# Kernel optimization log

Measured on AMD Instinct MI355X. Metric: run time of the kernel, lower is better.

## Reference

```python
import jax, jax.numpy as jnp
import numpy as np

D = 256; NH = 8; NL = 4; NP = 4; DFF = 1024
SHAPES = [(100, 100), (50, 50), (25, 25), (13, 13)]
B = 4


def layer_norm(x, g, b, eps=1e-5):
    m = x.mean(-1, keepdims=True)
    v = ((x - m) ** 2).mean(-1, keepdims=True)
    return (x - m) * jax.lax.rsqrt(v + eps) * g + b


def setup_inputs() -> dict:
    key = jax.random.key(0)
    ks = jax.random.split(key, 12)
    Lin = sum(h * w for h, w in SHAPES)  # 13294
    w = lambda k, s: jax.random.normal(k, s, jnp.float32) * 0.02
    return dict(
        src=jax.random.normal(ks[0], (B, Lin, D), jnp.float32),
        pos=0.1 * jax.random.normal(ks[1], (B, Lin, D), jnp.float32),
        reference_points=jax.random.uniform(ks[2], (B, Lin, NL, 2), dtype=jnp.float32),
        spatial_shapes=jnp.array(SHAPES, jnp.int32),
        level_start_index=jnp.array(np.cumsum([0] + [h * w for h, w in SHAPES])[:-1], jnp.int32),
        value_w=w(ks[3], (D, D)), value_b=jnp.zeros((D,), jnp.float32),
        offs_w=w(ks[4], (D, NH * NL * NP * 2)),
        offs_b=0.5 * jax.random.normal(ks[5], (NH * NL * NP * 2,), jnp.float32),
        attn_w=w(ks[6], (D, NH * NL * NP)), attn_b=jnp.zeros((NH * NL * NP,), jnp.float32),
        out_w=w(ks[7], (D, D)), out_b=jnp.zeros((D,), jnp.float32),
        ln1_g=jnp.ones((D,), jnp.float32), ln1_b=jnp.zeros((D,), jnp.float32),
        ff1_w=w(ks[8], (D, DFF)), ff1_b=jnp.zeros((DFF,), jnp.float32),
        ff2_w=w(ks[9], (DFF, D)), ff2_b=jnp.zeros((D,), jnp.float32),
        ln2_g=jnp.ones((D,), jnp.float32), ln2_b=jnp.zeros((D,), jnp.float32),
    )


def msda(query, value_in, ref, shapes, starts, value_w, value_b, offs_w, offs_b,
         attn_w, attn_b, out_w, out_b):
    Bq, Lq, Dm = query.shape
    dh = Dm // NH
    shapes_np = np.asarray(shapes); starts_np = np.asarray(starts)
    value = (value_in @ value_w + value_b).reshape(Bq, -1, NH, dh)
    offs = (query @ offs_w + offs_b).reshape(Bq, Lq, NH, NL, NP, 2)
    aw = jax.nn.softmax((query @ attn_w + attn_b).reshape(Bq, Lq, NH, NL * NP), axis=-1)
    aw = aw.reshape(Bq, Lq, NH, NL, NP)
    # offset normalizer is (W, H) per level
    normalizer = jnp.stack([shapes[:, 1], shapes[:, 0]], -1).astype(jnp.float32)
    loc = ref[:, :, None, :, None, :] + offs / normalizer[None, None, None, :, None, :]
    out = jnp.zeros((Bq, NH, Lq, dh), jnp.float32)
    for l in range(NL):
        Hl, Wl = int(shapes_np[l, 0]), int(shapes_np[l, 1])
        s = int(starts_np[l])
        v = value[:, s:s + Hl * Wl].transpose(0, 2, 1, 3)  # [B,h,HW,dh]
        x = loc[:, :, :, l, :, 0] * Wl - 0.5  # [B,Lq,h,P], align_corners=False
        y = loc[:, :, :, l, :, 1] * Hl - 0.5
        x0 = jnp.floor(x); y0 = jnp.floor(y)
        dx = x - x0; dy = y - y0
        x0i = x0.astype(jnp.int32); y0i = y0.astype(jnp.int32)
        def gather(ix, iy):
            valid = (ix >= 0) & (ix < Wl) & (iy >= 0) & (iy < Hl)  # zero padding
            idx = jnp.clip(iy, 0, Hl - 1) * Wl + jnp.clip(ix, 0, Wl - 1)
            idx = idx.transpose(0, 2, 1, 3).reshape(Bq, NH, Lq * NP)
            g = jnp.take_along_axis(v, idx[..., None], axis=2).reshape(Bq, NH, Lq, NP, dh)
            return g * valid.transpose(0, 2, 1, 3)[..., None]
        dxh = dx.transpose(0, 2, 1, 3)[..., None]
        dyh = dy.transpose(0, 2, 1, 3)[..., None]
        sampled = (gather(x0i, y0i) * (1 - dxh) * (1 - dyh)
                   + gather(x0i + 1, y0i) * dxh * (1 - dyh)
                   + gather(x0i, y0i + 1) * (1 - dxh) * dyh
                   + gather(x0i + 1, y0i + 1) * dxh * dyh)  # [B,h,Lq,P,dh]
        awl = aw[:, :, :, l].transpose(0, 2, 1, 3)[..., None]  # [B,h,Lq,P,1]
        out = out + (sampled * awl).sum(3)
    out = out.transpose(0, 2, 1, 3).reshape(Bq, Lq, Dm)
    return out @ out_w + out_b


def reference(src, pos, reference_points, spatial_shapes, level_start_index,
              value_w, value_b, offs_w, offs_b, attn_w, attn_b, out_w, out_b,
              ln1_g, ln1_b, ff1_w, ff1_b, ff2_w, ff2_b, ln2_g, ln2_b):
    # src = with_pos_embed(src, pos): NOTE this module uses (src + pos) as BOTH query and value
    q = src + pos
    src2 = msda(q, q, reference_points, spatial_shapes, level_start_index,
                value_w, value_b, offs_w, offs_b, attn_w, attn_b, out_w, out_b)
    x = layer_norm(q + src2, ln1_g, ln1_b)  # dropout is identity at eval
    ff = jnp.maximum(x @ ff1_w + ff1_b, 0.0) @ ff2_w + ff2_b
    return layer_norm(x + ff, ln2_g, ln2_b)
```

## Files before the change

### kernel.cpp

```cpp
#include <hip/hip_runtime.h>
#include <hip/hip_bf16.h>

#define B_    4
#define LIN   13294
#define M_    (B_*LIN)
#define D_    256
#define NH_   8
#define NL_   4
#define NP_   4
#define DFF_  1024

typedef __bf16 bf16;
typedef unsigned int uint;
typedef __attribute__((ext_vector_type(8))) __bf16 bfrag8;
typedef __attribute__((ext_vector_type(4))) __bf16 bf16x4;
typedef __attribute__((ext_vector_type(4))) float facc4;
typedef __attribute__((ext_vector_type(2))) float f32x2;

__global__ __launch_bounds__(256) void make_q(const float* __restrict__ src,
                                              const float* __restrict__ pos,
                                              float* __restrict__ q,
                                              bf16* __restrict__ qb, int n4) {
  int i = blockIdx.x * 256 + threadIdx.x;
  if (i >= n4) return;
  float4 s = ((const float4*)src)[i];
  float4 p = ((const float4*)pos)[i];
  float4 v = {s.x + p.x, s.y + p.y, s.z + p.z, s.w + p.w};
  ((float4*)q)[i] = v;
  bf16 t4[4] = {(bf16)v.x, (bf16)v.y, (bf16)v.z, (bf16)v.w};
  ((uint2*)qb)[i] = *(uint2*)t4;
}

__global__ __launch_bounds__(256) void prep_weights(
    const float* __restrict__ vw, const float* __restrict__ ow,
    const float* __restrict__ aw, const float* __restrict__ outw,
    const float* __restrict__ f1w, const float* __restrict__ f2w,
    const float* __restrict__ vb, const float* __restrict__ ob,
    const float* __restrict__ ab,
    bf16* __restrict__ vowt, bf16* __restrict__ outwt,
    bf16* __restrict__ f1wt, bf16* __restrict__ f2wt, float* __restrict__ vobias) {
  int seg = blockIdx.y;
  int idx = blockIdx.x * 256 + threadIdx.x;
  if (seg == 6) {
    if (idx < 256) vobias[idx] = vb[idx];
    else if (idx < 512) vobias[idx] = ob[idx - 256];
    else if (idx < 640) vobias[idx] = ab[idx - 512];
    return;
  }
  const float* W; bf16* Wt; int K, N;
  switch (seg) {
    case 0: W = vw;   Wt = vowt;              K = 256;  N = 256;  break;
    case 1: W = ow;   Wt = vowt + 256 * 256;  K = 256;  N = 256;  break;
    case 2: W = aw;   Wt = vowt + 512 * 256;  K = 256;  N = 128;  break;
    case 3: W = outw; Wt = outwt;             K = 256;  N = 256;  break;
    case 4: W = f1w;  Wt = f1wt;              K = 256;  N = 1024; break;
    default: W = f2w; Wt = f2wt;              K = 1024; N = 256;  break;
  }
  if (idx < K * N) {
    int n = idx / K, k = idx - n * K;
    Wt[idx] = (bf16)W[k * N + n];
  }
}

__device__ __forceinline__ void gload16(const bf16* g, bf16* l) {
  __builtin_amdgcn_global_load_lds(
      (const __attribute__((address_space(1))) uint*)g,
      (__attribute__((address_space(3))) uint*)l, 16, 0, 0);
}

template<int K, bool RELU>
__global__ __launch_bounds__(256) void gemm128(
    const bf16* __restrict__ A, const bf16* __restrict__ Bt,
    const float* __restrict__ bias, bf16* __restrict__ C,
    int Mdim, int N) {
  __shared__ __align__(16) bf16 As[128 * 64];
  __shared__ __align__(16) bf16 Bs[128 * 64];
  const int t = threadIdx.x, wave = t >> 6, lane = t & 63;
  const int m0 = blockIdx.x * 128, n0 = blockIdx.y * 128;
  const int wr = wave >> 1, wc = wave & 1;
  const int ln = lane & 15, quad = lane >> 4;
  const int sr = lane >> 3, cc = lane & 7;
  const int gcol = (cc ^ sr) * 8;

  const bf16* ap[4]; const bf16* bp[4];
  bf16* la[4]; bf16* lb[4];
  #pragma unroll
  for (int ii = 0; ii < 4; ii++) {
    int i = wave * 4 + ii;
    int arow = min(m0 + i * 8 + sr, Mdim - 1);
    ap[ii] = A + (size_t)arow * K + gcol;
    bp[ii] = Bt + (size_t)(n0 + i * 8 + sr) * K + gcol;
    la[ii] = As + i * 512;
    lb[ii] = Bs + i * 512;
  }
  int a_off[4], b_off[4];
  #pragma unroll
  for (int i = 0; i < 4; i++) {
    int ra = wr * 64 + i * 16 + ln;
    int rb = wc * 64 + i * 16 + ln;
    a_off[i] = ra * 128 + ((quad ^ (ra & 7)) * 16);
    b_off[i] = rb * 128 + ((quad ^ (rb & 7)) * 16);
  }

  facc4 acc[4][4];
  #pragma unroll
  for (int mt = 0; mt < 4; mt++)
    #pragma unroll
    for (int nt = 0; nt < 4; nt++) acc[mt][nt] = (facc4){0.f, 0.f, 0.f, 0.f};

  #pragma unroll 1
  for (int k0 = 0; k0 < K; k0 += 64) {
    __syncthreads();
    gload16(ap[0] + k0, la[0]); gload16(ap[1] + k0, la[1]);
    gload16(ap[2] + k0, la[2]); gload16(ap[3] + k0, la[3]);
    gload16(bp[0] + k0, lb[0]); gload16(bp[1] + k0, lb[1]);
    gload16(bp[2] + k0, lb[2]); gload16(bp[3] + k0, lb[3]);
    __syncthreads();
    #pragma unroll
    for (int ks = 0; ks < 2; ks++) {
      bfrag8 wfr[4], xfr[4];
      #pragma unroll
      for (int nt = 0; nt < 4; nt++)
        wfr[nt] = *(const bfrag8*)((const char*)Bs + (b_off[nt] ^ (ks * 64)));
      #pragma unroll
      for (int mt = 0; mt < 4; mt++)
        xfr[mt] = *(const bfrag8*)((const char*)As + (a_off[mt] ^ (ks * 64)));
      #pragma unroll
      for (int mt = 0; mt < 4; mt++)
        #pragma unroll
        for (int nt = 0; nt < 4; nt++)
          acc[mt][nt] = __builtin_amdgcn_mfma_f32_16x16x32_bf16(wfr[nt], xfr[mt], acc[mt][nt], 0, 0, 0);
    }
  }

  #pragma unroll
  for (int nt = 0; nt < 4; nt++) {
    int ncol = n0 + wc * 64 + nt * 16 + quad * 4;
    float4 bv = *(const float4*)&bias[ncol];
    #pragma unroll
    for (int mt = 0; mt < 4; mt++) {
      int row = m0 + wr * 64 + mt * 16 + ln;
      if (row < Mdim) {
        float v0 = acc[mt][nt][0] + bv.x, v1 = acc[mt][nt][1] + bv.y;
        float v2 = acc[mt][nt][2] + bv.z, v3 = acc[mt][nt][3] + bv.w;
        if (RELU) {
          v0 = fmaxf(v0, 0.f); v1 = fmaxf(v1, 0.f);
          v2 = fmaxf(v2, 0.f); v3 = fmaxf(v3, 0.f);
        }
        bf16 o[4] = {(bf16)v0, (bf16)v1, (bf16)v2, (bf16)v3};
        *(uint2*)&C[(size_t)row * N + ncol] = *(uint2*)o;
      }
    }
  }
}

__global__ __launch_bounds__(256) void msda_sample(
    const bf16* __restrict__ VOA,
    const float* __restrict__ ref,
    bf16* __restrict__ sampled) {
  int gw = (blockIdx.x * 256 + threadIdx.x) >> 6;
  int lane = threadIdx.x & 63;
  int m = gw >> 3, h = gw & 7;
  if (m >= M_) return;
  int b = m / LIN;
  int p = lane >> 2, cg = lane & 3;
  int l = p >> 2, pt = p & 3;
  int Wl = (l == 0) ? 100 : (l == 1) ? 50 : (l == 2) ? 25 : 13;
  int Hl = Wl;
  int st = (l == 0) ? 0 : (l == 1) ? 10000 : (l == 2) ? 12500 : 13125;

  const bf16* row = VOA + (size_t)m * 640;
  float e = __expf((float)row[512 + h * 16 + p]);
  float se = e;
  #pragma unroll
  for (int msk = 4; msk < 64; msk <<= 1) se += __shfl_xor(se, msk);
  float w = e / se;

  float rx = ref[((size_t)m * 4 + l) * 2 + 0];
  float ry = ref[((size_t)m * 4 + l) * 2 + 1];
  uint oxy = *(const uint*)&row[256 + ((h * 4 + l) * 4 + pt) * 2];
  float ox = __uint_as_float(oxy << 16);
  float oy = __uint_as_float(oxy & 0xffff0000u);
  float x = rx * (float)Wl + ox - 0.5f;
  float y = ry * (float)Hl + oy - 0.5f;
  float x0f = floorf(x), y0f = floorf(y);
  float dx = x - x0f, dy = y - y0f;
  int x0 = (int)x0f, y0 = (int)y0f;
  float wx1 = 1.f - dx, wy1 = 1.f - dy;

  f32x2 acc2[4];
  #pragma unroll
  for (int i = 0; i < 4; i++) acc2[i] = (f32x2){0.f, 0.f};

  size_t vbase = ((size_t)(b * LIN + st)) * 640 + h * 32 + cg * 8;
  #pragma unroll
  for (int c = 0; c < 4; c++) {
    int cx = c & 1, cy = c >> 1;
    int xi = x0 + cx, yi = y0 + cy;
    bool valid = (xi >= 0) & (xi < Wl) & (yi >= 0) & (yi < Hl);
    int xc = min(max(xi, 0), Wl - 1);
    int yc = min(max(yi, 0), Hl - 1);
    float cw = (cx ? dx : wx1) * (cy ? dy : wy1) * w;
    cw = valid ? cw : 0.f;
    uint off = (uint)(yc * Wl + xc) * 640u;
    const uint4 vv = *(const uint4*)(VOA + vbase + off);
    f32x2 cw2 = {cw, cw};
    f32x2 v0 = {__uint_as_float(vv.x << 16), __uint_as_float(vv.x & 0xffff0000u)};
    f32x2 v1 = {__uint_as_float(vv.y << 16), __uint_as_float(vv.y & 0xffff0000u)};
    f32x2 v2 = {__uint_as_float(vv.z << 16), __uint_as_float(vv.z & 0xffff0000u)};
    f32x2 v3 = {__uint_as_float(vv.w << 16), __uint_as_float(vv.w & 0xffff0000u)};
    acc2[0] = cw2 * v0 + acc2[0];
    acc2[1] = cw2 * v1 + acc2[1];
    acc2[2] = cw2 * v2 + acc2[2];
    acc2[3] = cw2 * v3 + acc2[3];
  }

  int sel = (lane >> 2) & 1;
  f32x2 sA0 = sel ? acc2[0] : acc2[2];
  f32x2 sA1 = sel ? acc2[1] : acc2[3];
  f32x2 kA0 = sel ? acc2[2] : acc2[0];
  f32x2 kA1 = sel ? acc2[3] : acc2[1];
  f32x2 rA0, rA1;
  rA0.x = __shfl_xor(sA0.x, 4); rA0.y = __shfl_xor(sA0.y, 4);
  rA1.x = __shfl_xor(sA1.x, 4); rA1.y = __shfl_xor(sA1.y, 4);
  kA0 += rA0; kA1 += rA1;

  int sel2 = (lane >> 3) & 1;
  f32x2 sB = sel2 ? kA0 : kA1;
  f32x2 kB = sel2 ? kA1 : kA0;
  f32x2 rB;
  rB.x = __shfl_xor(sB.x, 8); rB.y = __shfl_xor(sB.y, 8);
  kB += rB;

  int sel3 = (lane >> 4) & 1;
  float sC = sel3 ? kB.x : kB.y;
  float kC = sel3 ? kB.y : kB.x;
  kC += __shfl_xor(sC, 16);

  float v = kC + __shfl_xor(kC, 32);

  if (lane < 32) {
    int c = cg * 8 + ((lane >> 2) & 1) * 4 + ((lane >> 3) & 1) * 2 + ((lane >> 4) & 1);
    sampled[(size_t)m * 256 + h * 32 + c] = (bf16)v;
  }
}

__device__ inline float4 load4f(const float* p) { return *(const float4*)p; }
__device__ inline float4 load4f(const bf16* p) {
  bf16x4 v = *(const bf16x4*)p;
  float4 r = {(float)v[0], (float)v[1], (float)v[2], (float)v[3]};
  return r;
}
template<typename RT>
__global__ __launch_bounds__(256) void ln_kernel(
    const bf16* __restrict__ a, const RT* __restrict__ res,
    const float* __restrict__ g, const float* __restrict__ beta,
    float* __restrict__ out_f, bf16* __restrict__ out_b, int Mdim) {
  int wave = threadIdx.x >> 6, lane = threadIdx.x & 63;
  int row = blockIdx.x * 4 + wave;
  if (row >= Mdim) return;
  size_t base = (size_t)row * 256 + lane * 4;
  float4 av = load4f(a + base);
  float4 rv = load4f(res + base);
  float4 v = {av.x + rv.x, av.y + rv.y, av.z + rv.z, av.w + rv.w};
  float s = v.x + v.y + v.z + v.w;
  #pragma unroll
  for (int msk = 1; msk < 64; msk <<= 1) s += __shfl_xor(s, msk);
  float mean = s * (1.f / 256.f);
  float4 d = {v.x - mean, v.y - mean, v.z - mean, v.w - mean};
  float sq = d.x * d.x + d.y * d.y + d.z * d.z + d.w * d.w;
  #pragma unroll
  for (int msk = 1; msk < 64; msk <<= 1) sq += __shfl_xor(sq, msk);
  float inv = rsqrtf(sq * (1.f / 256.f) + 1e-5f);
  float4 gv = *(const float4*)(g + lane * 4);
  float4 bv = *(const float4*)(beta + lane * 4);
  float4 y = {d.x * inv * gv.x + bv.x, d.y * inv * gv.y + bv.y,
              d.z * inv * gv.z + bv.z, d.w * inv * gv.w + bv.w};
  if (out_f) *(float4*)(out_f + base) = y;
  if (out_b) {
    bf16 t4[4] = {(bf16)y.x, (bf16)y.y, (bf16)y.z, (bf16)y.w};
    *(uint2*)(out_b + base) = *(uint2*)t4;
  }
}

extern "C" void kernel_launch(void* const* d_in, const int* in_sizes, int n_in,
                              void* d_out, int out_size, void* d_ws, size_t ws_size,
                              hipStream_t stream) {
  const float* src     = (const float*)d_in[0];
  const float* pos     = (const float*)d_in[1];
  const float* refpts  = (const float*)d_in[2];
  const float* value_w = (const float*)d_in[5];
  const float* value_b = (const float*)d_in[6];
  const float* offs_w  = (const float*)d_in[7];
  const float* offs_b  = (const float*)d_in[8];
  const float* attn_w  = (const float*)d_in[9];
  const float* attn_b  = (const float*)d_in[10];
  const float* out_w   = (const float*)d_in[11];
  const float* out_b   = (const float*)d_in[12];
  const float* ln1_g   = (const float*)d_in[13];
  const float* ln1_b   = (const float*)d_in[14];
  const float* ff1_w   = (const float*)d_in[15];
  const float* ff1_b   = (const float*)d_in[16];
  const float* ff2_w   = (const float*)d_in[17];
  const float* ff2_b   = (const float*)d_in[18];
  const float* ln2_g   = (const float*)d_in[19];
  const float* ln2_b   = (const float*)d_in[20];

  char* ws = (char*)d_ws;
  size_t off = 0;
  auto take = [&](size_t bytes) -> char* {
    char* pp = ws + off;
    off += (bytes + 255) & ~(size_t)255;
    return pp;
  };
  float* q      = (float*)take((size_t)M_ * 256 * 4);
  size_t szQB   = (size_t)M_ * 256 * 2;
  size_t szVOA  = (size_t)M_ * 640 * 2;
  char* R       = take(szQB + szVOA + szQB);
  bf16* qb      = (bf16*)R;
  bf16* VOA     = (bf16*)(R + szQB);
  bf16* sampled = (bf16*)(R + szQB + szVOA);
  bf16* hb      = (bf16*)R;
  bf16* tmp     = (bf16*)take(szQB);
  bf16* x       = (bf16*)take(szQB);
  bf16* vowt    = (bf16*)take(640 * 256 * 2);
  bf16* outwt   = (bf16*)take(65536 * 2);
  bf16* f1wt    = (bf16*)take(262144 * 2);
  bf16* f2wt    = (bf16*)take(262144 * 2);
  float* vobias = (float*)take(640 * 4);
  (void)ws_size; (void)in_sizes; (void)n_in; (void)out_size;

  int n4 = M_ * 256 / 4;
  make_q<<<dim3((n4 + 255) / 256), dim3(256), 0, stream>>>(src, pos, q, qb, n4);
  prep_weights<<<dim3(1024, 7), dim3(256), 0, stream>>>(
      value_w, offs_w, attn_w, out_w, ff1_w, ff2_w, value_b, offs_b, attn_b,
      vowt, outwt, f1wt, f2wt, vobias);

  dim3 blk(256);
  int mt = (M_ + 127) / 128;
  gemm128<256, false><<<dim3(mt, 5), blk, 0, stream>>>(qb, vowt, vobias, VOA, M_, 640);
  msda_sample<<<dim3(M_ * 2), blk, 0, stream>>>(VOA, refpts, sampled);
  gemm128<256, false><<<dim3(mt, 2), blk, 0, stream>>>(sampled, outwt, out_b, tmp, M_, 256);
  ln_kernel<float><<<dim3((M_ + 3) / 4), blk, 0, stream>>>(tmp, q, ln1_g, ln1_b, nullptr, x, M_);
  gemm128<256, true><<<dim3(mt, 8), blk, 0, stream>>>(x, f1wt, ff1_b, hb, M_, 1024);
  gemm128<1024, false><<<dim3(mt, 2), blk, 0, stream>>>(hb, f2wt, ff2_b, tmp, M_, 256);
  ln_kernel<bf16><<<dim3((M_ + 3) / 4), blk, 0, stream>>>(tmp, x, ln2_g, ln2_b, (float*)d_out, nullptr, M_);
}
```

Baseline: 590.0 us.

## Assign one bilinear corner per lane and reduce sampled values through LDS

Each lane of the MSDA sampling kernel now handles one bilinear corner of one sample point. It loads the full 32-channel head slice as four 16-byte loads, where before each lane covered an 8-channel group across all four corners. Partial products go to a padded shared-memory buffer, are summed by column reads, and then reduced across lanes with xor shuffles. The aim is to cut the serial dependent gather loop and the select-heavy shuffle reduction, and to make each lane's loads contiguous. The cost is LDS traffic, a bigger per-lane register footprint, and inline waitcnt asm that relies on wave-synchronous execution.

```diff
diff --git a/kernel.cpp b/kernel.cpp
--- a/kernel.cpp
+++ b/kernel.cpp
@@ -154,16 +154,49 @@
   }
 }
 
+__device__ __forceinline__ f32x2 bfpair(uint u, f32x2 s) {
+  f32x2 r = {__uint_as_float(u << 16), __uint_as_float(u & 0xffff0000u)};
+  return r * s;
+}
+
+__device__ __forceinline__ void msda_phase(
+    uint4 A, uint4 B, f32x2 cw2, float* lrow, const float* rb,
+    bf16* outp, int lane) {
+  f32x2* lp = (f32x2*)lrow;
+  lp[0] = bfpair(A.x, cw2); lp[1] = bfpair(A.y, cw2);
+  lp[2] = bfpair(A.z, cw2); lp[3] = bfpair(A.w, cw2);
+  lp[4] = bfpair(B.x, cw2); lp[5] = bfpair(B.y, cw2);
+  lp[6] = bfpair(B.z, cw2); lp[7] = bfpair(B.w, cw2);
+  asm volatile("s_waitcnt lgkmcnt(0)" ::: "memory");
+  f32x2 s0 = *(const f32x2*)(rb + 0 * 18) + *(const f32x2*)(rb + 1 * 18);
+  f32x2 s1 = *(const f32x2*)(rb + 2 * 18) + *(const f32x2*)(rb + 3 * 18);
+  f32x2 s2 = *(const f32x2*)(rb + 4 * 18) + *(const f32x2*)(rb + 5 * 18);
+  f32x2 s3 = *(const f32x2*)(rb + 6 * 18) + *(const f32x2*)(rb + 7 * 18);
+  f32x2 s = (s0 + s1) + (s2 + s3);
+  #pragma unroll
+  for (int msk = 8; msk < 64; msk <<= 1) {
+    s.x += __shfl_xor(s.x, msk);
+    s.y += __shfl_xor(s.y, msk);
+  }
+  if (lane < 8) {
+    bf16 t2[2] = {(bf16)s.x, (bf16)s.y};
+    *(uint*)(outp + lane * 2) = *(uint*)t2;
+  }
+  asm volatile("" ::: "memory");
+}
+
 __global__ __launch_bounds__(256) void msda_sample(
     const bf16* __restrict__ VOA,
     const float* __restrict__ ref,
     bf16* __restrict__ sampled) {
+  __shared__ __align__(16) float red[4][64][18];
+  int wave = threadIdx.x >> 6;
   int gw = (blockIdx.x * 256 + threadIdx.x) >> 6;
   int lane = threadIdx.x & 63;
   int m = gw >> 3, h = gw & 7;
   if (m >= M_) return;
   int b = m / LIN;
-  int p = lane >> 2, cg = lane & 3;
+  int p = lane >> 2, corner = lane & 3;
   int l = p >> 2, pt = p & 3;
   int Wl = (l == 0) ? 100 : (l == 1) ? 50 : (l == 2) ? 25 : 13;
   int Hl = Wl;
@@ -176,73 +209,35 @@
   for (int msk = 4; msk < 64; msk <<= 1) se += __shfl_xor(se, msk);
   float w = e / se;
 
-  float rx = ref[((size_t)m * 4 + l) * 2 + 0];
-  float ry = ref[((size_t)m * 4 + l) * 2 + 1];
+  f32x2 rxy = *(const f32x2*)&ref[((size_t)m * 4 + l) * 2];
   uint oxy = *(const uint*)&row[256 + ((h * 4 + l) * 4 + pt) * 2];
   float ox = __uint_as_float(oxy << 16);
   float oy = __uint_as_float(oxy & 0xffff0000u);
-  float x = rx * (float)Wl + ox - 0.5f;
-  float y = ry * (float)Hl + oy - 0.5f;
+  float x = rxy.x * (float)Wl + ox - 0.5f;
+  float y = rxy.y * (float)Hl + oy - 0.5f;
   float x0f = floorf(x), y0f = floorf(y);
   float dx = x - x0f, dy = y - y0f;
-  int x0 = (int)x0f, y0 = (int)y0f;
-  float wx1 = 1.f - dx, wy1 = 1.f - dy;
-
-  f32x2 acc2[4];
-  #pragma unroll
-  for (int i = 0; i < 4; i++) acc2[i] = (f32x2){0.f, 0.f};
-
-  size_t vbase = ((size_t)(b * LIN + st)) * 640 + h * 32 + cg * 8;
-  #pragma unroll
-  for (int c = 0; c < 4; c++) {
-    int cx = c & 1, cy = c >> 1;
-    int xi = x0 + cx, yi = y0 + cy;
-    bool valid = (xi >= 0) & (xi < Wl) & (yi >= 0) & (yi < Hl);
-    int xc = min(max(xi, 0), Wl - 1);
-    int yc = min(max(yi, 0), Hl - 1);
-    float cw = (cx ? dx : wx1) * (cy ? dy : wy1) * w;
-    cw = valid ? cw : 0.f;
-    uint off = (uint)(yc * Wl + xc) * 640u;
-    const uint4 vv = *(const uint4*)(VOA + vbase + off);
-    f32x2 cw2 = {cw, cw};
-    f32x2 v0 = {__uint_as_float(vv.x << 16), __uint_as_float(vv.x & 0xffff0000u)};
-    f32x2 v1 = {__uint_as_float(vv.y << 16), __uint_as_float(vv.y & 0xffff0000u)};
-    f32x2 v2 = {__uint_as_float(vv.z << 16), __uint_as_float(vv.z & 0xffff0000u)};
-    f32x2 v3 = {__uint_as_float(vv.w << 16), __uint_as_float(vv.w & 0xffff0000u)};
-    acc2[0] = cw2 * v0 + acc2[0];
-    acc2[1] = cw2 * v1 + acc2[1];
-    acc2[2] = cw2 * v2 + acc2[2];
-    acc2[3] = cw2 * v3 + acc2[3];
-  }
-
-  int sel = (lane >> 2) & 1;
-  f32x2 sA0 = sel ? acc2[0] : acc2[2];
-  f32x2 sA1 = sel ? acc2[1] : acc2[3];
-  f32x2 kA0 = sel ? acc2[2] : acc2[0];
-  f32x2 kA1 = sel ? acc2[3] : acc2[1];
-  f32x2 rA0, rA1;
-  rA0.x = __shfl_xor(sA0.x, 4); rA0.y = __shfl_xor(sA0.y, 4);
-  rA1.x = __shfl_xor(sA1.x, 4); rA1.y = __shfl_xor(sA1.y, 4);
-  kA0 += rA0; kA1 += rA1;
-
-  int sel2 = (lane >> 3) & 1;
-  f32x2 sB = sel2 ? kA0 : kA1;
-  f32x2 kB = sel2 ? kA1 : kA0;
-  f32x2 rB;
-  rB.x = __shfl_xor(sB.x, 8); rB.y = __shfl_xor(sB.y, 8);
-  kB += rB;
-
-  int sel3 = (lane >> 4) & 1;
-  float sC = sel3 ? kB.x : kB.y;
-  float kC = sel3 ? kB.y : kB.x;
-  kC += __shfl_xor(sC, 16);
-
-  float v = kC + __shfl_xor(kC, 32);
-
-  if (lane < 32) {
-    int c = cg * 8 + ((lane >> 2) & 1) * 4 + ((lane >> 3) & 1) * 2 + ((lane >> 4) & 1);
-    sampled[(size_t)m * 256 + h * 32 + c] = (bf16)v;
-  }
+  int cx = corner & 1, cy = corner >> 1;
+  int xi = (int)x0f + cx, yi = (int)y0f + cy;
+  bool valid = (xi >= 0) & (xi < Wl) & (yi >= 0) & (yi < Hl);
+  int xc = min(max(xi, 0), Wl - 1);
+  int yc = min(max(yi, 0), Hl - 1);
+  float cw = (cx ? dx : 1.f - dx) * (cy ? dy : 1.f - dy) * w;
+  cw = valid ? cw : 0.f;
+
+  const bf16* vp = VOA + ((size_t)(b * LIN + st) + (size_t)(yc * Wl + xc)) * 640 + h * 32;
+  uint4 va = *(const uint4*)(vp);
+  uint4 vb = *(const uint4*)(vp + 8);
+  uint4 vc = *(const uint4*)(vp + 16);
+  uint4 vd = *(const uint4*)(vp + 24);
+
+  f32x2 cw2 = {cw, cw};
+  float* lrow = &red[wave][lane][0];
+  const float* rb = &red[wave][(lane >> 3) * 8][0] + (lane & 7) * 2;
+  bf16* outp = sampled + (size_t)m * 256 + h * 32;
+
+  msda_phase(va, vb, cw2, lrow, rb, outp, lane);
+  msda_phase(vc, vd, cw2, lrow, rb, outp + 16, lane);
 }
 
 __device__ inline float4 load4f(const float* p) { return *(const float4*)p; }
```

Result: slower. 631.5 us (+7.0%).

## Double-buffer GEMM LDS tiles with K=32 stages and async prefetch

Applied to the files above, without the earlier changes.

Restructures the bf16 MFMA GEMM main loop from single-buffered 64-wide K tiles into two 32-wide LDS buffers. The global-to-LDS load for stage t+2 is issued while stage t+1 is still arriving, with explicit vmcnt waits and barriers. The LDS layout and swizzle change to pack two rows per 128-byte line. The goal is to hide global load latency behind MFMA work, at the cost of more barriers per K step and trickier hand-written synchronisation.

```diff
diff --git a/kernel.cpp b/kernel.cpp
--- a/kernel.cpp
+++ b/kernel.cpp
@@ -73,33 +73,33 @@
     const bf16* __restrict__ A, const bf16* __restrict__ Bt,
     const float* __restrict__ bias, bf16* __restrict__ C,
     int Mdim, int N) {
-  __shared__ __align__(16) bf16 As[128 * 64];
-  __shared__ __align__(16) bf16 Bs[128 * 64];
+  __shared__ __align__(16) bf16 As[2][4096];
+  __shared__ __align__(16) bf16 Bs[2][4096];
   const int t = threadIdx.x, wave = t >> 6, lane = t & 63;
   const int m0 = blockIdx.x * 128, n0 = blockIdx.y * 128;
   const int wr = wave >> 1, wc = wave & 1;
   const int ln = lane & 15, quad = lane >> 4;
-  const int sr = lane >> 3, cc = lane & 7;
-  const int gcol = (cc ^ sr) * 8;
-
-  const bf16* ap[4]; const bf16* bp[4];
-  bf16* la[4]; bf16* lb[4];
-  #pragma unroll
-  for (int ii = 0; ii < 4; ii++) {
-    int i = wave * 4 + ii;
-    int arow = min(m0 + i * 8 + sr, Mdim - 1);
-    ap[ii] = A + (size_t)arow * K + gcol;
-    bp[ii] = Bt + (size_t)(n0 + i * 8 + sr) * K + gcol;
-    la[ii] = As + i * 512;
-    lb[ii] = Bs + i * 512;
+
+  const bf16* ap[2]; const bf16* bp[2];
+  int sdst[2];
+  #pragma unroll
+  for (int j = 0; j < 2; j++) {
+    int s = wave * 2 + j;
+    int L = s * 8 + (lane >> 3);
+    int lc = (lane & 7) ^ (L & 7);
+    int r = 2 * L + (lc >> 2);
+    int kq = (lc & 3) * 8;
+    ap[j] = A + (size_t)min(m0 + r, Mdim - 1) * K + kq;
+    bp[j] = Bt + (size_t)(n0 + r) * K + kq;
+    sdst[j] = s * 512;
   }
   int a_off[4], b_off[4];
   #pragma unroll
   for (int i = 0; i < 4; i++) {
     int ra = wr * 64 + i * 16 + ln;
     int rb = wc * 64 + i * 16 + ln;
-    a_off[i] = ra * 128 + ((quad ^ (ra & 7)) * 16);
-    b_off[i] = rb * 128 + ((quad ^ (rb & 7)) * 16);
+    a_off[i] = (ra >> 1) * 128 + (((((ra & 1) << 2) | quad) ^ ((ra >> 1) & 7)) * 16);
+    b_off[i] = (rb >> 1) * 128 + (((((rb & 1) << 2) | quad) ^ ((rb >> 1) & 7)) * 16);
   }
 
   facc4 acc[4][4];
@@ -108,28 +108,52 @@
     #pragma unroll
     for (int nt = 0; nt < 4; nt++) acc[mt][nt] = (facc4){0.f, 0.f, 0.f, 0.f};
 
+  constexpr int NT = K / 32;
+  gload16(ap[0] + 0,  As[0] + sdst[0]);
+  gload16(ap[1] + 0,  As[0] + sdst[1]);
+  gload16(bp[0] + 0,  Bs[0] + sdst[0]);
+  gload16(bp[1] + 0,  Bs[0] + sdst[1]);
+  gload16(ap[0] + 32, As[1] + sdst[0]);
+  gload16(ap[1] + 32, As[1] + sdst[1]);
+  gload16(bp[0] + 32, Bs[1] + sdst[0]);
+  gload16(bp[1] + 32, Bs[1] + sdst[1]);
+  asm volatile("s_waitcnt vmcnt(4)" ::: "memory");
+  __builtin_amdgcn_s_barrier();
+  asm volatile("" ::: "memory");
+
   #pragma unroll 1
-  for (int k0 = 0; k0 < K; k0 += 64) {
-    __syncthreads();
-    gload16(ap[0] + k0, la[0]); gload16(ap[1] + k0, la[1]);
-    gload16(ap[2] + k0, la[2]); gload16(ap[3] + k0, la[3]);
-    gload16(bp[0] + k0, lb[0]); gload16(bp[1] + k0, lb[1]);
-    gload16(bp[2] + k0, lb[2]); gload16(bp[3] + k0, lb[3]);
-    __syncthreads();
-    #pragma unroll
-    for (int ks = 0; ks < 2; ks++) {
-      bfrag8 wfr[4], xfr[4];
+  for (int tt = 0; tt < NT; ++tt) {
+    const char* ab = (const char*)As[tt & 1];
+    const char* bb = (const char*)Bs[tt & 1];
+    bfrag8 wfr[4], xfr[4];
+    #pragma unroll
+    for (int nt = 0; nt < 4; nt++)
+      wfr[nt] = *(const bfrag8*)(bb + b_off[nt]);
+    #pragma unroll
+    for (int mt = 0; mt < 4; mt++)
+      xfr[mt] = *(const bfrag8*)(ab + a_off[mt]);
+    #pragma unroll
+    for (int mt = 0; mt < 4; mt++)
       #pragma unroll
       for (int nt = 0; nt < 4; nt++)
-        wfr[nt] = *(const bfrag8*)((const char*)Bs + (b_off[nt] ^ (ks * 64)));
-      #pragma unroll
-      for (int mt = 0; mt < 4; mt++)
-        xfr[mt] = *(const bfrag8*)((const char*)As + (a_off[mt] ^ (ks * 64)));
-      #pragma unroll
-      for (int mt = 0; mt < 4; mt++)
-        #pragma unroll
-        for (int nt = 0; nt < 4; nt++)
-          acc[mt][nt] = __builtin_amdgcn_mfma_f32_16x16x32_bf16(wfr[nt], xfr[mt], acc[mt][nt], 0, 0, 0);
+        acc[mt][nt] = __builtin_amdgcn_mfma_f32_16x16x32_bf16(wfr[nt], xfr[mt], acc[mt][nt], 0, 0, 0);
+
+    if (tt + 2 < NT) {
+      asm volatile("" ::: "memory");
+      __builtin_amdgcn_s_barrier();
+      int kk = (tt + 2) * 32;
+      bf16* la = As[tt & 1]; bf16* lb = Bs[tt & 1];
+      gload16(ap[0] + kk, la + sdst[0]);
+      gload16(ap[1] + kk, la + sdst[1]);
+      gload16(bp[0] + kk, lb + sdst[0]);
+      gload16(bp[1] + kk, lb + sdst[1]);
+      asm volatile("s_waitcnt vmcnt(4)" ::: "memory");
+      __builtin_amdgcn_s_barrier();
+      asm volatile("" ::: "memory");
+    } else if (tt + 1 < NT) {
+      asm volatile("s_waitcnt vmcnt(0)" ::: "memory");
+      __builtin_amdgcn_s_barrier();
+      asm volatile("" ::: "memory");
     }
   }
 
```

Result: no change. 596.0 us (+1.0%).

## Replace LDS-staged GEMM with register-direct global loads into MFMA

Applied to the files above, without the earlier changes.

The shared-memory tiled GEMM (128x128 tile, global_load_lds plus barriers) is replaced by a kernel where each wave loads its A and B fragments straight from global memory into registers, 256 K-elements at a time, and issues MFMAs with no LDS or __syncthreads. The block tile becomes 64 rows by 128 columns, split across waves by column. This removes barrier and LDS traffic, but every wave re-reads the same A rows from global/L2 with little sharing, and register pressure rises sharply.

```diff
diff --git a/kernel.cpp b/kernel.cpp
--- a/kernel.cpp
+++ b/kernel.cpp
@@ -62,84 +62,65 @@
   }
 }
 
-__device__ __forceinline__ void gload16(const bf16* g, bf16* l) {
-  __builtin_amdgcn_global_load_lds(
-      (const __attribute__((address_space(1))) uint*)g,
-      (__attribute__((address_space(3))) uint*)l, 16, 0, 0);
-}
-
 template<int K, bool RELU>
-__global__ __launch_bounds__(256) void gemm128(
+__global__ __launch_bounds__(256) void gemm_rw(
     const bf16* __restrict__ A, const bf16* __restrict__ Bt,
     const float* __restrict__ bias, bf16* __restrict__ C,
     int Mdim, int N) {
-  __shared__ __align__(16) bf16 As[128 * 64];
-  __shared__ __align__(16) bf16 Bs[128 * 64];
-  const int t = threadIdx.x, wave = t >> 6, lane = t & 63;
-  const int m0 = blockIdx.x * 128, n0 = blockIdx.y * 128;
-  const int wr = wave >> 1, wc = wave & 1;
+  const int wave = threadIdx.x >> 6, lane = threadIdx.x & 63;
   const int ln = lane & 15, quad = lane >> 4;
-  const int sr = lane >> 3, cc = lane & 7;
-  const int gcol = (cc ^ sr) * 8;
-
-  const bf16* ap[4]; const bf16* bp[4];
-  bf16* la[4]; bf16* lb[4];
-  #pragma unroll
-  for (int ii = 0; ii < 4; ii++) {
-    int i = wave * 4 + ii;
-    int arow = min(m0 + i * 8 + sr, Mdim - 1);
-    ap[ii] = A + (size_t)arow * K + gcol;
-    bp[ii] = Bt + (size_t)(n0 + i * 8 + sr) * K + gcol;
-    la[ii] = As + i * 512;
-    lb[ii] = Bs + i * 512;
-  }
-  int a_off[4], b_off[4];
-  #pragma unroll
-  for (int i = 0; i < 4; i++) {
-    int ra = wr * 64 + i * 16 + ln;
-    int rb = wc * 64 + i * 16 + ln;
-    a_off[i] = ra * 128 + ((quad ^ (ra & 7)) * 16);
-    b_off[i] = rb * 128 + ((quad ^ (rb & 7)) * 16);
-  }
-
-  facc4 acc[4][4];
+  const int m0 = blockIdx.x * 64;
+  const int n0 = blockIdx.y * 128 + wave * 32;
+
+  const bf16* bp0 = Bt + (size_t)(n0 + ln) * K + quad * 8;
+  const bf16* bp1 = bp0 + (size_t)16 * K;
+  const bf16* ap[4];
   #pragma unroll
   for (int mt = 0; mt < 4; mt++)
+    ap[mt] = A + (size_t)min(m0 + mt * 16 + ln, Mdim - 1) * K + quad * 8;
+
+  facc4 acc[4][2];
+  #pragma unroll
+  for (int mt = 0; mt < 4; mt++) {
+    acc[mt][0] = (facc4){0.f, 0.f, 0.f, 0.f};
+    acc[mt][1] = (facc4){0.f, 0.f, 0.f, 0.f};
+  }
+
+  constexpr int NC = K / 256;
+  #pragma unroll 1
+  for (int kc = 0; kc < NC; kc++) {
+    bfrag8 bf0[8], bf1[8];
     #pragma unroll
-    for (int nt = 0; nt < 4; nt++) acc[mt][nt] = (facc4){0.f, 0.f, 0.f, 0.f};
-
-  #pragma unroll 1
-  for (int k0 = 0; k0 < K; k0 += 64) {
-    __syncthreads();
-    gload16(ap[0] + k0, la[0]); gload16(ap[1] + k0, la[1]);
-    gload16(ap[2] + k0, la[2]); gload16(ap[3] + k0, la[3]);
-    gload16(bp[0] + k0, lb[0]); gload16(bp[1] + k0, lb[1]);
-    gload16(bp[2] + k0, lb[2]); gload16(bp[3] + k0, lb[3]);
-    __syncthreads();
+    for (int ks = 0; ks < 8; ks++) {
+      bf0[ks] = *(const bfrag8*)(bp0 + ks * 32);
+      bf1[ks] = *(const bfrag8*)(bp1 + ks * 32);
+    }
     #pragma unroll
-    for (int ks = 0; ks < 2; ks++) {
-      bfrag8 wfr[4], xfr[4];
+    for (int mt = 0; mt < 4; mt++) {
+      bfrag8 af[8];
       #pragma unroll
-      for (int nt = 0; nt < 4; nt++)
-        wfr[nt] = *(const bfrag8*)((const char*)Bs + (b_off[nt] ^ (ks * 64)));
+      for (int ks = 0; ks < 8; ks++)
+        af[ks] = *(const bfrag8*)(ap[mt] + ks * 32);
       #pragma unroll
-      for (int mt = 0; mt < 4; mt++)
-        xfr[mt] = *(const bfrag8*)((const char*)As + (a_off[mt] ^ (ks * 64)));
+      for (int ks = 0; ks < 8; ks++) {
+        acc[mt][0] = __builtin_amdgcn_mfma_f32_16x16x32_bf16(bf0[ks], af[ks], acc[mt][0], 0, 0, 0);
+        acc[mt][1] = __builtin_amdgcn_mfma_f32_16x16x32_bf16(bf1[ks], af[ks], acc[mt][1], 0, 0, 0);
+      }
+    }
+    if (NC > 1) {
+      bp0 += 256; bp1 += 256;
       #pragma unroll
-      for (int mt = 0; mt < 4; mt++)
-        #pragma unroll
-        for (int nt = 0; nt < 4; nt++)
-          acc[mt][nt] = __builtin_amdgcn_mfma_f32_16x16x32_bf16(wfr[nt], xfr[mt], acc[mt][nt], 0, 0, 0);
+      for (int mt = 0; mt < 4; mt++) ap[mt] += 256;
     }
   }
 
   #pragma unroll
-  for (int nt = 0; nt < 4; nt++) {
-    int ncol = n0 + wc * 64 + nt * 16 + quad * 4;
+  for (int nt = 0; nt < 2; nt++) {
+    int ncol = n0 + nt * 16 + quad * 4;
     float4 bv = *(const float4*)&bias[ncol];
     #pragma unroll
     for (int mt = 0; mt < 4; mt++) {
-      int row = m0 + wr * 64 + mt * 16 + ln;
+      int row = m0 + mt * 16 + ln;
       if (row < Mdim) {
         float v0 = acc[mt][nt][0] + bv.x, v1 = acc[mt][nt][1] + bv.y;
         float v2 = acc[mt][nt][2] + bv.z, v3 = acc[mt][nt][3] + bv.w;
@@ -337,12 +318,12 @@
       vowt, outwt, f1wt, f2wt, vobias);
 
   dim3 blk(256);
-  int mt = (M_ + 127) / 128;
-  gemm128<256, false><<<dim3(mt, 5), blk, 0, stream>>>(qb, vowt, vobias, VOA, M_, 640);
+  int mb = (M_ + 63) / 64;
+  gemm_rw<256, false><<<dim3(mb, 5), blk, 0, stream>>>(qb, vowt, vobias, VOA, M_, 640);
   msda_sample<<<dim3(M_ * 2), blk, 0, stream>>>(VOA, refpts, sampled);
-  gemm128<256, false><<<dim3(mt, 2), blk, 0, stream>>>(sampled, outwt, out_b, tmp, M_, 256);
+  gemm_rw<256, false><<<dim3(mb, 2), blk, 0, stream>>>(sampled, outwt, out_b, tmp, M_, 256);
   ln_kernel<float><<<dim3((M_ + 3) / 4), blk, 0, stream>>>(tmp, q, ln1_g, ln1_b, nullptr, x, M_);
-  gemm128<256, true><<<dim3(mt, 8), blk, 0, stream>>>(x, f1wt, ff1_b, hb, M_, 1024);
-  gemm128<1024, false><<<dim3(mt, 2), blk, 0, stream>>>(hb, f2wt, ff2_b, tmp, M_, 256);
+  gemm_rw<256, true><<<dim3(mb, 8), blk, 0, stream>>>(x, f1wt, ff1_b, hb, M_, 1024);
+  gemm_rw<1024, false><<<dim3(mb, 2), blk, 0, stream>>>(hb, f2wt, ff2_b, tmp, M_, 256);
   ln_kernel<bf16><<<dim3((M_ + 3) / 4), blk, 0, stream>>>(tmp, x, ln2_g, ln2_b, (float*)d_out, nullptr, M_);
 }
```

After: 808.1 us. 1.37x slower.
